# Performance work log

Measured on AMD Instinct MI355X. Metric: run time of the kernel, lower is better.

Reference implementation:

```python
import jax, jax.numpy as jnp
import numpy as np

B, H, S, D = 4, 16, 2048, 64


def setup_inputs() -> dict:
    key = jax.random.key(0)
    kq, kk, kv = jax.random.split(key, 3)
    q = jax.random.normal(kq, (B, H, S, D), dtype=jnp.float32)
    k = jax.random.normal(kk, (B, H, S, D), dtype=jnp.float32)
    v = jax.random.normal(kv, (B, H, S, D), dtype=jnp.float32)
    return {"q": q, "k": k, "v": v, "num_k": 170}


def reference(q, k, v, num_k):
    d_tensor = k.shape[-1]
    # [B,H,S,S] score matrix
    score = jnp.einsum("bhqd,bhkd->bhqk", q, k) / jnp.sqrt(jnp.float32(d_tensor))
    nk = min(int(num_k), k.shape[2])
    if nk:
        # kth-largest value per query row acts as threshold
        top_vals = jax.lax.top_k(score, nk)[0]          # [B,H,S,nk]
        thresh = top_vals[..., -1:]                      # [B,H,S,1]
        score = jnp.where(score < thresh, jnp.float32(-1e18), score)
    attn = jax.nn.softmax(score, axis=-1)
    return jnp.einsum("bhqk,bhkd->bhqd", attn, v)
```

## Files before the change

### kernel.cpp

```cpp
#include <hip/hip_runtime.h>
#include <math.h>

#define S_LEN 2048
#define DHEAD 64
#define NBINS 512
#define BPL (NBINS / 64)
#define CANDMAX 48
#define NBH 64
#define NROWS (NBH * S_LEN)
#define VT_BYTES (64ull * DHEAD * S_LEN * 2)

typedef _Float16 f16x8 __attribute__((ext_vector_type(8)));
typedef _Float16 f16x4 __attribute__((ext_vector_type(4)));
typedef float    f32x4 __attribute__((ext_vector_type(4)));

__global__ __launch_bounds__(256)
void prep_vt(const float* __restrict__ V, _Float16* __restrict__ VT) {
  const int bh  = (int)blockIdx.x >> 3;
  const int dg8 = (int)blockIdx.x & 7;
  const int t   = (int)threadIdx.x;
  const int dim = dg8 * 8 + (t >> 5);
  const int kc  = t & 31;
  const float* Vb = V + (size_t)bh * (S_LEN * DHEAD);
  _Float16* VTb = VT + ((size_t)bh * DHEAD + dim) * S_LEN;
  for (int i = 0; i < 8; ++i) {
    int key0 = (kc + i * 32) * 8;
    f16x8 h;
    #pragma unroll
    for (int j = 0; j < 8; ++j)
      h[j] = (_Float16)Vb[(size_t)(key0 + j) * DHEAD + dim];
    *(f16x8*)(VTb + key0) = h;
  }
}

__global__ __launch_bounds__(256, 4)
void qk_kernel(const float* __restrict__ Q, const float* __restrict__ K,
               float* __restrict__ Sws, int row0) {
  __shared__ __align__(16) char kbuf[32768];
  f16x8* Khw = (f16x8*)kbuf;
  f16x8* Klw = (f16x8*)(kbuf + 16384);

  const int tid  = (int)threadIdx.x;
  const int lane = tid & 63;
  const int wid  = tid >> 6;
  const int nxl  = (int)gridDim.x >> 3;
  const int xcd  = (int)blockIdx.x & 7;
  const int lb   = (int)blockIdx.x >> 3;
  const int rb   = lb >> 2;
  const int kb   = lb & 3;
  const int rowl = xcd * (nxl * 16) + rb * 64 + wid * 16;
  const int rowg = row0 + rowl;
  const int bh   = rowg >> 11;
  const int key0 = kb * 512;

  const int g = lane >> 4;
  const int m = lane & 15;

  f16x8 a_hi0, a_lo0, a_hi1, a_lo1;
  {
    const float* Qrow = Q + (size_t)(rowg + m) * DHEAD;
    float4 qa = *(const float4*)(Qrow + g * 8);
    float4 qb = *(const float4*)(Qrow + g * 8 + 4);
    float4 qc = *(const float4*)(Qrow + 32 + g * 8);
    float4 qd = *(const float4*)(Qrow + 32 + g * 8 + 4);
    float x[16] = {qa.x,qa.y,qa.z,qa.w, qb.x,qb.y,qb.z,qb.w,
                   qc.x,qc.y,qc.z,qc.w, qd.x,qd.y,qd.z,qd.w};
    #pragma unroll
    for (int j = 0; j < 8; ++j) {
      _Float16 h0 = (_Float16)x[j];
      a_hi0[j] = h0;  a_lo0[j] = (_Float16)(x[j] - (float)h0);
      _Float16 h1 = (_Float16)x[8 + j];
      a_hi1[j] = h1;  a_lo1[j] = (_Float16)(x[8 + j] - (float)h1);
    }
  }

  const float* Kb = K + (size_t)bh * (S_LEN * DHEAD);
  float* Srow = Sws + (size_t)rowl * S_LEN;

  const int skey  = tid >> 1;
  const int shalf = tid & 1;
  const int ssw   = skey & 7;

  float4 pf[8];
  {
    const float4* kr = (const float4*)(Kb + (size_t)(key0 + skey) * DHEAD + shalf * 32);
    #pragma unroll
    for (int j = 0; j < 8; ++j) pf[j] = kr[j];
  }

  for (int t = 0; t < 4; ++t) {
    #pragma unroll
    for (int jj = 0; jj < 4; ++jj) {
      float x[8] = {pf[2*jj].x, pf[2*jj].y, pf[2*jj].z, pf[2*jj].w,
                    pf[2*jj+1].x, pf[2*jj+1].y, pf[2*jj+1].z, pf[2*jj+1].w};
      f16x8 hi, lo;
      #pragma unroll
      for (int j = 0; j < 8; ++j) {
        _Float16 h = (_Float16)x[j];
        hi[j] = h;
        lo[j] = (_Float16)(x[j] - (float)h);
      }
      int c = shalf * 4 + jj;
      Khw[skey * 8 + (c ^ ssw)] = hi;
      Klw[skey * 8 + (c ^ ssw)] = lo;
    }
    if (t + 1 < 4) {
      const float4* kr = (const float4*)(Kb + (size_t)(key0 + (t + 1) * 128 + skey) * DHEAD + shalf * 32);
      #pragma unroll
      for (int j = 0; j < 8; ++j) pf[j] = kr[j];
    }
    __syncthreads();

    const f16x8* Kh = (const f16x8*)kbuf;
    const f16x8* Kl = (const f16x8*)(kbuf + 16384);
    int slot0 = ( g      ^ (m & 7));
    int slot1 = ((4 + g) ^ (m & 7));
    #pragma unroll
    for (int p = 0; p < 8; ++p) {
      int keyr = p * 16 + m;
      f16x8 b_hi0 = Kh[keyr * 8 + slot0];
      f16x8 b_hi1 = Kh[keyr * 8 + slot1];
      f16x8 b_lo0 = Kl[keyr * 8 + slot0];
      f16x8 b_lo1 = Kl[keyr * 8 + slot1];
      f32x4 acc = {0.f, 0.f, 0.f, 0.f};
      acc = __builtin_amdgcn_mfma_f32_16x16x32_f16(a_hi0, b_hi0, acc, 0, 0, 0);
      acc = __builtin_amdgcn_mfma_f32_16x16x32_f16(a_hi1, b_hi1, acc, 0, 0, 0);
      acc = __builtin_amdgcn_mfma_f32_16x16x32_f16(a_hi0, b_lo0, acc, 0, 0, 0);
      acc = __builtin_amdgcn_mfma_f32_16x16x32_f16(a_hi1, b_lo1, acc, 0, 0, 0);
      acc = __builtin_amdgcn_mfma_f32_16x16x32_f16(a_lo0, b_hi0, acc, 0, 0, 0);
      acc = __builtin_amdgcn_mfma_f32_16x16x32_f16(a_lo1, b_hi1, acc, 0, 0, 0);
      acc = __builtin_amdgcn_mfma_f32_16x16x32_f16(a_lo0, b_lo0, acc, 0, 0, 0);
      acc = __builtin_amdgcn_mfma_f32_16x16x32_f16(a_lo1, b_lo1, acc, 0, 0, 0);
      int col = key0 + t * 128 + p * 16 + m;
      #pragma unroll
      for (int rg = 0; rg < 4; ++rg)
        __builtin_nontemporal_store(acc[rg] * 0.125f,
            &Srow[(size_t)(g * 4 + rg) * S_LEN + col]);
    }
    __syncthreads();
  }
}

__global__ __launch_bounds__(512, 4)
void selmm_kernel(const float* __restrict__ Sws, const _Float16* __restrict__ VT,
                  const int* __restrict__ nkp, float* __restrict__ Out, int row0) {
  __shared__ __align__(16) char pbuf[65536];
  __shared__ __align__(16) float4 redS[4][64];
  __shared__ float psumS[16];
  __shared__ unsigned candCnt[8];
  unsigned* histS = (unsigned*)pbuf;
  float*    candA = (float*)(pbuf + 16384);

  const int tid  = (int)threadIdx.x;
  const int lane = tid & 63;
  const int wid  = tid >> 6;
  const int nxl  = (int)gridDim.x >> 3;
  const int xcd  = (int)blockIdx.x & 7;
  const int lbk  = (int)blockIdx.x >> 3;
  const int rowlb = xcd * (nxl * 16) + lbk * 16;
  const int rowgb = row0 + rowlb;
  const int bh    = rowgb >> 11;

  int nk = nkp[0];
  if (nk > S_LEN) nk = S_LEN;

  unsigned* hw = histS + wid * NBINS;
  float*    cw = candA + wid * CANDMAX;
  float sarr[2][32];
  float thr2[2], vmx2[2];

  #pragma unroll
  for (int rr = 0; rr < 2; ++rr) {
    const int rloc = wid * 2 + rr;
    {
      const f32x4* S4 = (const f32x4*)(Sws + (size_t)(rowlb + rloc) * S_LEN);
      #pragma unroll
      for (int j = 0; j < 8; ++j) {
        f32x4 v4 = __builtin_nontemporal_load(S4 + j * 64 + lane);
        sarr[rr][j*4+0] = v4[0]; sarr[rr][j*4+1] = v4[1];
        sarr[rr][j*4+2] = v4[2]; sarr[rr][j*4+3] = v4[3];
      }
    }

    float vmax = -INFINITY, vmin = INFINITY;
    #pragma unroll
    for (int q = 0; q < 32; ++q) {
      vmax = fmaxf(vmax, sarr[rr][q]); vmin = fminf(vmin, sarr[rr][q]);
    }
    #pragma unroll
    for (int off = 32; off >= 1; off >>= 1) {
      vmax = fmaxf(vmax, __shfl_xor(vmax, off));
      vmin = fminf(vmin, __shfl_xor(vmin, off));
    }

    float thresh = -INFINITY;
    if (nk > 0) {
      float range = vmax - vmin;
      float scale = (range > 0.f) ? ((float)NBINS / range) : 0.f;
      float boff  = vmin * scale;

      #pragma unroll
      for (int i2 = 0; i2 < BPL; ++i2) hw[(i2 << 6) | lane] = 0u;
      #pragma unroll
      for (int q = 0; q < 32; ++q) {
        int bb = (int)fmaf(sarr[rr][q], scale, -boff);
        bb = bb < 0 ? 0 : (bb > NBINS - 1 ? NBINS - 1 : bb);
        atomicAdd(&hw[((bb & 7) << 6) | (bb >> 3)], 1u);
      }

      unsigned A = 0;
      #pragma unroll
      for (int i2 = 0; i2 < BPL; ++i2) A += hw[(i2 << 6) | lane];
      unsigned ssum = A;
      #pragma unroll
      for (int off = 1; off <= 32; off <<= 1) {
        unsigned u = (unsigned)__shfl_down((int)ssum, off);
        if (lane + off < 64) ssum += u;
      }
      unsigned cum = ssum - A;
      int bsel = -1; int mloc = 0; int nbloc = 0;
      #pragma unroll
      for (int i2 = BPL - 1; i2 >= 0; --i2) {
        unsigned c0 = cum; cum += hw[(i2 << 6) | lane];
        if (bsel < 0 && c0 < (unsigned)nk && cum >= (unsigned)nk) {
          bsel = (lane << 3) | i2; mloc = nk - (int)c0; nbloc = (int)(cum - c0);
        }
      }
      unsigned long long fm = __ballot(bsel >= 0);
      int srcl = __ffsll(fm) - 1;
      bsel = __shfl(bsel, srcl);
      int mth  = __shfl(mloc, srcl);
      int nbin = __shfl(nbloc, srcl);

      if (nbin <= CANDMAX) {
        if (lane == 0) candCnt[wid] = 0u;
        __builtin_amdgcn_wave_barrier();
        #pragma unroll
        for (int q = 0; q < 32; ++q) {
          int bb = (int)fmaf(sarr[rr][q], scale, -boff);
          bb = bb < 0 ? 0 : (bb > NBINS - 1 ? NBINS - 1 : bb);
          if (bb == bsel) {
            unsigned ix = atomicAdd(&candCnt[wid], 1u);
            if (ix < CANDMAX) cw[ix] = sarr[rr][q];
          }
        }
        __builtin_amdgcn_wave_barrier();
        float prev = INFINITY, kth = -INFINITY;
        int got = 0, guard = 0;
        while (got < mth && guard++ <= CANDMAX) {
          float best = -INFINITY;
          for (int i = 0; i < nbin; ++i) {
            float v = cw[i];
            if (v < prev && v > best) best = v;
          }
          int ce = 0;
          for (int i = 0; i < nbin; ++i) if (cw[i] == best) ce++;
          got += ce; prev = best; kth = best;
        }
        thresh = kth;
      } else {
        unsigned inbin = 0;
        #pragma unroll
        for (int q = 0; q < 32; ++q) {
          int bb = (int)fmaf(sarr[rr][q], scale, -boff);
          bb = bb < 0 ? 0 : (bb > NBINS - 1 ? NBINS - 1 : bb);
          if (bb == bsel) inbin |= (1u << q);
        }
        while (true) {
          float cmax = -INFINITY;
          #pragma unroll
          for (int q = 0; q < 32; ++q) if (inbin & (1u << q)) cmax = fmaxf(cmax, sarr[rr][q]);
          #pragma unroll
          for (int off = 32; off >= 1; off >>= 1) cmax = fmaxf(cmax, __shfl_xor(cmax, off));
          int cnt = 0;
          #pragma unroll
          for (int q = 0; q < 32; ++q) if ((inbin & (1u << q)) && sarr[rr][q] == cmax) cnt++;
          #pragma unroll
          for (int off = 32; off >= 1; off >>= 1) cnt += __shfl_xor(cnt, off);
          if (mth <= cnt) { thresh = cmax; break; }
          mth -= cnt;
          #pragma unroll
          for (int q = 0; q < 32; ++q) if ((inbin & (1u << q)) && sarr[rr][q] == cmax) inbin &= ~(1u << q);
        }
      }
    }
    thr2[rr] = thresh; vmx2[rr] = vmax;

    float psum = 0.f;
    #pragma unroll
    for (int q = 0; q < 32; ++q) {
      float s = sarr[rr][q];
      psum += (s >= thresh) ? __expf(s - vmax) : 0.f;
    }
    #pragma unroll
    for (int off = 32; off >= 1; off >>= 1) psum += __shfl_xor(psum, off);
    if (lane == 0) psumS[rloc] = psum;
  }
  __syncthreads();

  #pragma unroll
  for (int rr = 0; rr < 2; ++rr) {
    const int row = wid * 2 + rr;
    const int swz = (row & 7) << 4;
    #pragma unroll
    for (int j = 0; j < 8; ++j) {
      f16x4 pv;
      #pragma unroll
      for (int c = 0; c < 4; ++c) {
        float s = sarr[rr][j*4+c];
        pv[c] = (_Float16)((s >= thr2[rr]) ? __expf(s - vmx2[rr]) : 0.f);
      }
      *(f16x4*)(pbuf + ((row * 4096 + j * 512 + lane * 8) ^ swz)) = pv;
    }
  }
  __syncthreads();

  const int g    = lane >> 4;
  const int n16  = lane & 15;
  const int dg   = wid & 3;
  const int kh   = wid >> 2;
  const int swzA = (n16 & 7) << 4;
  const _Float16* VTb = VT + (size_t)bh * (DHEAD * S_LEN);
  f32x4 acc = {0.f, 0.f, 0.f, 0.f};

  #pragma unroll
  for (int kt = 0; kt < 8; ++kt) {
    #pragma unroll
    for (int s = 0; s < 4; ++s) {
      f16x8 af = *(const f16x8*)(pbuf +
          ((n16 * 4096 + kt * 512 + kh * 256 + s * 64 + g * 16) ^ swzA));
      f16x8 bf = *(const f16x8*)(VTb + (size_t)(dg * 16 + n16) * S_LEN +
                                 kt * 256 + kh * 128 + s * 32 + g * 8);
      acc = __builtin_amdgcn_mfma_f32_16x16x32_f16(af, bf, acc, 0, 0, 0);
    }
  }

  if (kh == 1) {
    redS[dg][lane] = make_float4(acc[0], acc[1], acc[2], acc[3]);
  }
  __syncthreads();
  if (kh == 0) {
    float4 o = redS[dg][lane];
    float ov[4] = {o.x, o.y, o.z, o.w};
    #pragma unroll
    for (int rg = 0; rg < 4; ++rg) {
      int row = g * 4 + rg;
      float val = (acc[rg] + ov[rg]) / psumS[row];
      Out[(size_t)(rowgb + row) * DHEAD + dg * 16 + n16] = val;
    }
  }
}

#define TQ 16
#define KT 128
#define NTILES (S_LEN / KT)
#define THREADS 512
#define LCAP 256
#define SOFF   0
#define KHI    131072
#define KLO    147456
#define HOFF   131072
#define KLOFF  147456
#define PLOFF  155648

__global__ __launch_bounds__(THREADS, 2)
void dpsa_kernel(const float* __restrict__ Q, const float* __restrict__ K,
                 const float* __restrict__ V, const int* __restrict__ nkp,
                 float* __restrict__ Out) {
  __shared__ __align__(16) char smem[163840];
  float* Sf = (float*)(smem + SOFF);

  const int tid  = (int)threadIdx.x;
  const int lane = tid & 63;
  const int wid  = tid >> 6;
  const int bid  = (int)blockIdx.x;
  const int bh   = bid >> 7;
  const int qblk = bid & 127;
  const size_t base = (size_t)bh * (size_t)(S_LEN * DHEAD);
  const float* Kbh = K + base;
  const float* Vbh = V + base;

  int nk = nkp[0];
  if (nk > S_LEN) nk = S_LEN;

  const int g = lane >> 4;
  const int m = lane & 15;

  f16x8 a_hi0, a_lo0, a_hi1, a_lo1;
  {
    const float* Qrow = Q + base + (size_t)(qblk * TQ + m) * DHEAD;
    float4 qa = *(const float4*)(Qrow + g * 8);
    float4 qb = *(const float4*)(Qrow + g * 8 + 4);
    float4 qc = *(const float4*)(Qrow + 32 + g * 8);
    float4 qd = *(const float4*)(Qrow + 32 + g * 8 + 4);
    float x[16] = {qa.x,qa.y,qa.z,qa.w, qb.x,qb.y,qb.z,qb.w,
                   qc.x,qc.y,qc.z,qc.w, qd.x,qd.y,qd.z,qd.w};
    #pragma unroll
    for (int j = 0; j < 8; ++j) {
      _Float16 h0 = (_Float16)x[j];
      a_hi0[j] = h0;  a_lo0[j] = (_Float16)(x[j] - (float)h0);
      _Float16 h1 = (_Float16)x[8 + j];
      a_hi1[j] = h1;  a_lo1[j] = (_Float16)(x[8 + j] - (float)h1);
    }
  }

  const f16x8* Kh = (const f16x8*)(smem + KHI);
  const f16x8* Kl = (const f16x8*)(smem + KLO);
  const int keyl = tid >> 2;
  const int q4i  = tid & 3;
  const int sw   = keyl & 7;

  float4 pf0, pf1, pf2, pf3;
  {
    const float4* Kg4 = (const float4*)Kbh;
    int idx = keyl * 16 + q4i * 4;
    pf0 = Kg4[idx]; pf1 = Kg4[idx + 1]; pf2 = Kg4[idx + 2]; pf3 = Kg4[idx + 3];
  }

  for (int t = 0; t < NTILES; ++t) {
    {
      float x[16] = {pf0.x,pf0.y,pf0.z,pf0.w, pf1.x,pf1.y,pf1.z,pf1.w,
                     pf2.x,pf2.y,pf2.z,pf2.w, pf3.x,pf3.y,pf3.z,pf3.w};
      f16x8 hi0, hi1, lo0, lo1;
      #pragma unroll
      for (int j = 0; j < 8; ++j) {
        _Float16 h0 = (_Float16)x[j];
        hi0[j] = h0;  lo0[j] = (_Float16)(x[j] - (float)h0);
        _Float16 h1 = (_Float16)x[8 + j];
        hi1[j] = h1;  lo1[j] = (_Float16)(x[8 + j] - (float)h1);
      }
      f16x8* KhwF = (f16x8*)(smem + KHI);
      f16x8* KlwF = (f16x8*)(smem + KLO);
      KhwF[keyl * 8 + ((q4i * 2)     ^ sw)] = hi0;
      KhwF[keyl * 8 + ((q4i * 2 + 1) ^ sw)] = hi1;
      KlwF[keyl * 8 + ((q4i * 2)     ^ sw)] = lo0;
      KlwF[keyl * 8 + ((q4i * 2 + 1) ^ sw)] = lo1;
    }
    if (t + 1 < NTILES) {
      const float4* Kg4 = (const float4*)(Kbh + (size_t)(t + 1) * (KT * DHEAD));
      int idx = keyl * 16 + q4i * 4;
      pf0 = Kg4[idx]; pf1 = Kg4[idx + 1]; pf2 = Kg4[idx + 2]; pf3 = Kg4[idx + 3];
    }
    __syncthreads();
    {
      int keyr = wid * 16 + m;
      int s0 = ( g      ^ (m & 7));
      int s1 = ((4 + g) ^ (m & 7));
      f16x8 b_hi0 = Kh[keyr * 8 + s0];
      f16x8 b_hi1 = Kh[keyr * 8 + s1];
      f16x8 b_lo0 = Kl[keyr * 8 + s0];
      f16x8 b_lo1 = Kl[keyr * 8 + s1];
      f32x4 acc = {0.f, 0.f, 0.f, 0.f};
      acc = __builtin_amdgcn_mfma_f32_16x16x32_f16(a_hi0, b_hi0, acc, 0, 0, 0);
      acc = __builtin_amdgcn_mfma_f32_16x16x32_f16(a_hi1, b_hi1, acc, 0, 0, 0);
      acc = __builtin_amdgcn_mfma_f32_16x16x32_f16(a_hi0, b_lo0, acc, 0, 0, 0);
      acc = __builtin_amdgcn_mfma_f32_16x16x32_f16(a_hi1, b_lo1, acc, 0, 0, 0);
      acc = __builtin_amdgcn_mfma_f32_16x16x32_f16(a_lo0, b_hi0, acc, 0, 0, 0);
      acc = __builtin_amdgcn_mfma_f32_16x16x32_f16(a_lo1, b_hi1, acc, 0, 0, 0);
      int keyabs = t * KT + wid * 16 + m;
      #pragma unroll
      for (int rg = 0; rg < 4; ++rg)
        Sf[(size_t)(g * 4 + rg) * S_LEN + keyabs] = acc[rg] * 0.125f;
    }
    __syncthreads();
  }

  unsigned* hw = (unsigned*)(smem + HOFF)  + wid * NBINS;
  unsigned* kl = (unsigned*)(smem + KLOFF) + wid * LCAP;
  float*    pl = (float*)(smem + PLOFF)    + wid * LCAP;
  const float4* S4 = (const float4*)(smem + SOFF);

  for (int rr = 0; rr < 2; ++rr) {
    const int row = wid * 2 + rr;
    float sarr[32];
    #pragma unroll
    for (int j = 0; j < 8; ++j) {
      float4 v4 = S4[row * (S_LEN / 4) + j * 64 + lane];
      sarr[j*4+0] = v4.x; sarr[j*4+1] = v4.y;
      sarr[j*4+2] = v4.z; sarr[j*4+3] = v4.w;
    }

    float vmax = -INFINITY, vmin = INFINITY;
    #pragma unroll
    for (int q = 0; q < 32; ++q) {
      vmax = fmaxf(vmax, sarr[q]); vmin = fminf(vmin, sarr[q]);
    }
    #pragma unroll
    for (int off = 32; off >= 1; off >>= 1) {
      vmax = fmaxf(vmax, __shfl_xor(vmax, off));
      vmin = fminf(vmin, __shfl_xor(vmin, off));
    }

    float thresh = -INFINITY;
    if (nk > 0) {
      float range = vmax - vmin;
      float scale = (range > 0.f) ? ((float)NBINS / range) : 0.f;
      #pragma unroll
      for (int i2 = 0; i2 < BPL; ++i2) hw[(i2 << 6) | lane] = 0u;
      #pragma unroll
      for (int q = 0; q < 32; ++q) {
        int bb = (int)((sarr[q] - vmin) * scale);
        bb = bb < 0 ? 0 : (bb > NBINS - 1 ? NBINS - 1 : bb);
        atomicAdd(&hw[((bb & 7) << 6) | (bb >> 3)], 1u);
      }
      unsigned A = 0; unsigned hv[BPL];
      #pragma unroll
      for (int i2 = 0; i2 < BPL; ++i2) { hv[i2] = hw[(i2 << 6) | lane]; A += hv[i2]; }
      unsigned ssum = A;
      #pragma unroll
      for (int off = 1; off <= 32; off <<= 1) {
        unsigned u = (unsigned)__shfl_down((int)ssum, off);
        if (lane + off < 64) ssum += u;
      }
      unsigned cum = ssum - A;
      int bsel = -1; int mloc = 0;
      #pragma unroll
      for (int i2 = BPL - 1; i2 >= 0; --i2) {
        unsigned c0 = cum; cum += hv[i2];
        if (bsel < 0 && c0 < (unsigned)nk && cum >= (unsigned)nk) {
          bsel = (lane << 3) | i2; mloc = nk - (int)c0;
        }
      }
      unsigned long long fm = __ballot(bsel >= 0);
      int srcl = __ffsll(fm) - 1;
      bsel = __shfl(bsel, srcl);
      int mth = __shfl(mloc, srcl);

      unsigned inbin = 0;
      #pragma unroll
      for (int q = 0; q < 32; ++q) {
        int bb = (int)((sarr[q] - vmin) * scale);
        bb = bb < 0 ? 0 : (bb > NBINS - 1 ? NBINS - 1 : bb);
        if (bb == bsel) inbin |= (1u << q);
      }
      while (true) {
        float cmax = -INFINITY;
        #pragma unroll
        for (int q = 0; q < 32; ++q) if (inbin & (1u << q)) cmax = fmaxf(cmax, sarr[q]);
        #pragma unroll
        for (int off = 32; off >= 1; off >>= 1) cmax = fmaxf(cmax, __shfl_xor(cmax, off));
        int cnt = 0;
        #pragma unroll
        for (int q = 0; q < 32; ++q) if ((inbin & (1u << q)) && sarr[q] == cmax) cnt++;
        #pragma unroll
        for (int off = 32; off >= 1; off >>= 1) cnt += __shfl_xor(cnt, off);
        if (mth <= cnt) { thresh = cmax; break; }
        mth -= cnt;
        #pragma unroll
        for (int q = 0; q < 32; ++q) if ((inbin & (1u << q)) && sarr[q] == cmax) inbin &= ~(1u << q);
      }
    }

    float psum = 0.f;
    #pragma unroll
    for (int q = 0; q < 32; ++q) {
      float p = (sarr[q] >= thresh) ? expf(sarr[q] - vmax) : 0.f;
      sarr[q] = p; psum += p;
    }
    #pragma unroll
    for (int off = 32; off >= 1; off >>= 1) psum += __shfl_xor(psum, off);

    unsigned nkept = 0;
    #pragma unroll
    for (int q = 0; q < 32; ++q) {
      bool keep = sarr[q] > 0.f;
      unsigned long long mk = __ballot(keep);
      if (keep) {
        unsigned idx = nkept + (unsigned)__popcll(mk & ((1ull << lane) - 1ull));
        if (idx < LCAP) {
          kl[idx] = (unsigned)((q >> 2) * 256 + lane * 4 + (q & 3));
          pl[idx] = sarr[q];
        }
      }
      nkept += (unsigned)__popcll(mk);
    }

    float acc0 = 0.f, acc1 = 0.f, acc2 = 0.f, acc3 = 0.f;
    if (nkept <= LCAP) {
      unsigned i = 0;
      for (; i + 4 <= nkept; i += 4) {
        acc0 = fmaf(pl[i+0], Vbh[(size_t)kl[i+0] * DHEAD + lane], acc0);
        acc1 = fmaf(pl[i+1], Vbh[(size_t)kl[i+1] * DHEAD + lane], acc1);
        acc2 = fmaf(pl[i+2], Vbh[(size_t)kl[i+2] * DHEAD + lane], acc2);
        acc3 = fmaf(pl[i+3], Vbh[(size_t)kl[i+3] * DHEAD + lane], acc3);
      }
      for (; i < nkept; ++i)
        acc0 = fmaf(pl[i], Vbh[(size_t)kl[i] * DHEAD + lane], acc0);
    } else {
      #pragma unroll
      for (int q = 0; q < 32; ++q) {
        for (int sl = 0; sl < 64; ++sl) {
          float pp = __shfl(sarr[q], sl);
          if (pp > 0.f)
            acc0 = fmaf(pp, Vbh[(size_t)((q >> 2) * 256 + sl * 4 + (q & 3)) * DHEAD + lane], acc0);
        }
      }
    }
    float accv = (acc0 + acc1) + (acc2 + acc3);
    Out[base + (size_t)(qblk * TQ + row) * DHEAD + lane] = accv / psum;
  }
}

extern "C" void kernel_launch(void* const* d_in, const int* in_sizes, int n_in,
                              void* d_out, int out_size, void* d_ws, size_t ws_size,
                              hipStream_t stream) {
  const float* q  = (const float*)d_in[0];
  const float* k  = (const float*)d_in[1];
  const float* v  = (const float*)d_in[2];
  const int*   nk = (const int*)d_in[3];
  float* out = (float*)d_out;

  size_t srem = (ws_size > VT_BYTES) ? (ws_size - VT_BYTES) : 0;
  size_t maxrows = srem / ((size_t)S_LEN * sizeof(float));
  long long chunk = (long long)(maxrows / 512) * 512;
  if (chunk > NROWS) chunk = NROWS;

  if (chunk >= 512) {
    _Float16* vt = (_Float16*)d_ws;
    float* sws = (float*)((char*)d_ws + VT_BYTES);
    prep_vt<<<dim3(512), dim3(256), 0, stream>>>(v, vt);
    for (int row0 = 0; row0 < NROWS; row0 += (int)chunk) {
      int rows = (NROWS - row0 < (int)chunk) ? (NROWS - row0) : (int)chunk;
      qk_kernel<<<dim3(rows / 16), dim3(256), 0, stream>>>(q, k, sws, row0);
      selmm_kernel<<<dim3(rows / 16), dim3(512), 0, stream>>>(sws, vt, nk, out, row0);
    }
  } else {
    dpsa_kernel<<<dim3(8192), dim3(THREADS), 0, stream>>>(q, k, v, nk, out);
  }
}
```

Measured before the change: 988.8 us.

## Process 8 rows per selmm block, one row per wave, to cut registers and LDS

The selection+PV kernel now assigns one score row per wave (8 rows per block) instead of two, halving the per-thread score array and shrinking LDS from 64KB to 36KB. The grid doubles to keep coverage. The 16-row MFMA tile is padded with a zeroed row, so half the PV MFMA work and V loads per block are wasted. The aim is higher occupancy and more latency hiding in the memory-bound selection phase, paid for with duplicated V reads.

```diff
diff --git a/kernel.cpp b/kernel.cpp
--- a/kernel.cpp
+++ b/kernel.cpp
@@ -144,9 +144,9 @@
 __global__ __launch_bounds__(512, 4)
 void selmm_kernel(const float* __restrict__ Sws, const _Float16* __restrict__ VT,
                   const int* __restrict__ nkp, float* __restrict__ Out, int row0) {
-  __shared__ __align__(16) char pbuf[65536];
+  __shared__ __align__(16) char pbuf[36864];
   __shared__ __align__(16) float4 redS[4][64];
-  __shared__ float psumS[16];
+  __shared__ float psumS[8];
   __shared__ unsigned candCnt[8];
   unsigned* histS = (unsigned*)pbuf;
   float*    candA = (float*)(pbuf + 16384);
@@ -157,7 +157,7 @@
   const int nxl  = (int)gridDim.x >> 3;
   const int xcd  = (int)blockIdx.x & 7;
   const int lbk  = (int)blockIdx.x >> 3;
-  const int rowlb = xcd * (nxl * 16) + lbk * 16;
+  const int rowlb = xcd * (nxl * 8) + lbk * 8;
   const int rowgb = row0 + rowlb;
   const int bh    = rowgb >> 11;
 
@@ -166,151 +166,153 @@
 
   unsigned* hw = histS + wid * NBINS;
   float*    cw = candA + wid * CANDMAX;
-  float sarr[2][32];
-  float thr2[2], vmx2[2];
-
+  float sarr[32];
+  float thr, vmx;
+
+  {
+    const f32x4* S4 = (const f32x4*)(Sws + (size_t)(rowlb + wid) * S_LEN);
+    #pragma unroll
+    for (int j = 0; j < 8; ++j) {
+      f32x4 v4 = __builtin_nontemporal_load(S4 + j * 64 + lane);
+      sarr[j*4+0] = v4[0]; sarr[j*4+1] = v4[1];
+      sarr[j*4+2] = v4[2]; sarr[j*4+3] = v4[3];
+    }
+  }
+
+  float vmax = -INFINITY, vmin = INFINITY;
   #pragma unroll
-  for (int rr = 0; rr < 2; ++rr) {
-    const int rloc = wid * 2 + rr;
-    {
-      const f32x4* S4 = (const f32x4*)(Sws + (size_t)(rowlb + rloc) * S_LEN);
-      #pragma unroll
-      for (int j = 0; j < 8; ++j) {
-        f32x4 v4 = __builtin_nontemporal_load(S4 + j * 64 + lane);
-        sarr[rr][j*4+0] = v4[0]; sarr[rr][j*4+1] = v4[1];
-        sarr[rr][j*4+2] = v4[2]; sarr[rr][j*4+3] = v4[3];
-      }
-    }
-
-    float vmax = -INFINITY, vmin = INFINITY;
+  for (int q = 0; q < 32; ++q) {
+    vmax = fmaxf(vmax, sarr[q]); vmin = fminf(vmin, sarr[q]);
+  }
+  #pragma unroll
+  for (int off = 32; off >= 1; off >>= 1) {
+    vmax = fmaxf(vmax, __shfl_xor(vmax, off));
+    vmin = fminf(vmin, __shfl_xor(vmin, off));
+  }
+
+  float thresh = -INFINITY;
+  if (nk > 0) {
+    float range = vmax - vmin;
+    float scale = (range > 0.f) ? ((float)NBINS / range) : 0.f;
+    float boff  = vmin * scale;
+
+    #pragma unroll
+    for (int i2 = 0; i2 < BPL; ++i2) hw[(i2 << 6) | lane] = 0u;
     #pragma unroll
     for (int q = 0; q < 32; ++q) {
-      vmax = fmaxf(vmax, sarr[rr][q]); vmin = fminf(vmin, sarr[rr][q]);
-    }
-    #pragma unroll
-    for (int off = 32; off >= 1; off >>= 1) {
-      vmax = fmaxf(vmax, __shfl_xor(vmax, off));
-      vmin = fminf(vmin, __shfl_xor(vmin, off));
-    }
-
-    float thresh = -INFINITY;
-    if (nk > 0) {
-      float range = vmax - vmin;
-      float scale = (range > 0.f) ? ((float)NBINS / range) : 0.f;
-      float boff  = vmin * scale;
-
-      #pragma unroll
-      for (int i2 = 0; i2 < BPL; ++i2) hw[(i2 << 6) | lane] = 0u;
+      int bb = (int)fmaf(sarr[q], scale, -boff);
+      bb = bb < 0 ? 0 : (bb > NBINS - 1 ? NBINS - 1 : bb);
+      atomicAdd(&hw[((bb & 7) << 6) | (bb >> 3)], 1u);
+    }
+
+    unsigned A = 0;
+    #pragma unroll
+    for (int i2 = 0; i2 < BPL; ++i2) A += hw[(i2 << 6) | lane];
+    unsigned ssum = A;
+    #pragma unroll
+    for (int off = 1; off <= 32; off <<= 1) {
+      unsigned u = (unsigned)__shfl_down((int)ssum, off);
+      if (lane + off < 64) ssum += u;
+    }
+    unsigned cum = ssum - A;
+    int bsel = -1; int mloc = 0; int nbloc = 0;
+    #pragma unroll
+    for (int i2 = BPL - 1; i2 >= 0; --i2) {
+      unsigned c0 = cum; cum += hw[(i2 << 6) | lane];
+      if (bsel < 0 && c0 < (unsigned)nk && cum >= (unsigned)nk) {
+        bsel = (lane << 3) | i2; mloc = nk - (int)c0; nbloc = (int)(cum - c0);
+      }
+    }
+    unsigned long long fm = __ballot(bsel >= 0);
+    int srcl = __ffsll(fm) - 1;
+    bsel = __shfl(bsel, srcl);
+    int mth  = __shfl(mloc, srcl);
+    int nbin = __shfl(nbloc, srcl);
+
+    if (nbin <= CANDMAX) {
+      if (lane == 0) candCnt[wid] = 0u;
+      __builtin_amdgcn_wave_barrier();
       #pragma unroll
       for (int q = 0; q < 32; ++q) {
-        int bb = (int)fmaf(sarr[rr][q], scale, -boff);
+        int bb = (int)fmaf(sarr[q], scale, -boff);
         bb = bb < 0 ? 0 : (bb > NBINS - 1 ? NBINS - 1 : bb);
-        atomicAdd(&hw[((bb & 7) << 6) | (bb >> 3)], 1u);
-      }
-
-      unsigned A = 0;
-      #pragma unroll
-      for (int i2 = 0; i2 < BPL; ++i2) A += hw[(i2 << 6) | lane];
-      unsigned ssum = A;
-      #pragma unroll
-      for (int off = 1; off <= 32; off <<= 1) {
-        unsigned u = (unsigned)__shfl_down((int)ssum, off);
-        if (lane + off < 64) ssum += u;
-      }
-      unsigned cum = ssum - A;
-      int bsel = -1; int mloc = 0; int nbloc = 0;
-      #pragma unroll
-      for (int i2 = BPL - 1; i2 >= 0; --i2) {
-        unsigned c0 = cum; cum += hw[(i2 << 6) | lane];
-        if (bsel < 0 && c0 < (unsigned)nk && cum >= (unsigned)nk) {
-          bsel = (lane << 3) | i2; mloc = nk - (int)c0; nbloc = (int)(cum - c0);
+        if (bb == bsel) {
+          unsigned ix = atomicAdd(&candCnt[wid], 1u);
+          if (ix < CANDMAX) cw[ix] = sarr[q];
         }
       }
-      unsigned long long fm = __ballot(bsel >= 0);
-      int srcl = __ffsll(fm) - 1;
-      bsel = __shfl(bsel, srcl);
-      int mth  = __shfl(mloc, srcl);
-      int nbin = __shfl(nbloc, srcl);
-
-      if (nbin <= CANDMAX) {
-        if (lane == 0) candCnt[wid] = 0u;
-        __builtin_amdgcn_wave_barrier();
-        #pragma unroll
-        for (int q = 0; q < 32; ++q) {
-          int bb = (int)fmaf(sarr[rr][q], scale, -boff);
-          bb = bb < 0 ? 0 : (bb > NBINS - 1 ? NBINS - 1 : bb);
-          if (bb == bsel) {
-            unsigned ix = atomicAdd(&candCnt[wid], 1u);
-            if (ix < CANDMAX) cw[ix] = sarr[rr][q];
-          }
+      __builtin_amdgcn_wave_barrier();
+      float prev = INFINITY, kth = -INFINITY;
+      int got = 0, guard = 0;
+      while (got < mth && guard++ <= CANDMAX) {
+        float best = -INFINITY;
+        for (int i = 0; i < nbin; ++i) {
+          float v = cw[i];
+          if (v < prev && v > best) best = v;
         }
-        __builtin_amdgcn_wave_barrier();
-        float prev = INFINITY, kth = -INFINITY;
-        int got = 0, guard = 0;
-        while (got < mth && guard++ <= CANDMAX) {
-          float best = -INFINITY;
-          for (int i = 0; i < nbin; ++i) {
-            float v = cw[i];
-            if (v < prev && v > best) best = v;
-          }
-          int ce = 0;
-          for (int i = 0; i < nbin; ++i) if (cw[i] == best) ce++;
-          got += ce; prev = best; kth = best;
-        }
-        thresh = kth;
-      } else {
-        unsigned inbin = 0;
-        #pragma unroll
-        for (int q = 0; q < 32; ++q) {
-          int bb = (int)fmaf(sarr[rr][q], scale, -boff);
-          bb = bb < 0 ? 0 : (bb > NBINS - 1 ? NBINS - 1 : bb);
-          if (bb == bsel) inbin |= (1u << q);
-        }
-        while (true) {
-          float cmax = -INFINITY;
-          #pragma unroll
-          for (int q = 0; q < 32; ++q) if (inbin & (1u << q)) cmax = fmaxf(cmax, sarr[rr][q]);
-          #pragma unroll
-          for (int off = 32; off >= 1; off >>= 1) cmax = fmaxf(cmax, __shfl_xor(cmax, off));
-          int cnt = 0;
-          #pragma unroll
-          for (int q = 0; q < 32; ++q) if ((inbin & (1u << q)) && sarr[rr][q] == cmax) cnt++;
-          #pragma unroll
-          for (int off = 32; off >= 1; off >>= 1) cnt += __shfl_xor(cnt, off);
-          if (mth <= cnt) { thresh = cmax; break; }
-          mth -= cnt;
-          #pragma unroll
-          for (int q = 0; q < 32; ++q) if ((inbin & (1u << q)) && sarr[rr][q] == cmax) inbin &= ~(1u << q);
-        }
-      }
-    }
-    thr2[rr] = thresh; vmx2[rr] = vmax;
-
+        int ce = 0;
+        for (int i = 0; i < nbin; ++i) if (cw[i] == best) ce++;
+        got += ce; prev = best; kth = best;
+      }
+      thresh = kth;
+    } else {
+      unsigned inbin = 0;
+      #pragma unroll
+      for (int q = 0; q < 32; ++q) {
+        int bb = (int)fmaf(sarr[q], scale, -boff);
+        bb = bb < 0 ? 0 : (bb > NBINS - 1 ? NBINS - 1 : bb);
+        if (bb == bsel) inbin |= (1u << q);
+      }
+      while (true) {
+        float cmax = -INFINITY;
+        #pragma unroll
+        for (int q = 0; q < 32; ++q) if (inbin & (1u << q)) cmax = fmaxf(cmax, sarr[q]);
+        #pragma unroll
+        for (int off = 32; off >= 1; off >>= 1) cmax = fmaxf(cmax, __shfl_xor(cmax, off));
+        int cnt = 0;
+        #pragma unroll
+        for (int q = 0; q < 32; ++q) if ((inbin & (1u << q)) && sarr[q] == cmax) cnt++;
+        #pragma unroll
+        for (int off = 32; off >= 1; off >>= 1) cnt += __shfl_xor(cnt, off);
+        if (mth <= cnt) { thresh = cmax; break; }
+        mth -= cnt;
+        #pragma unroll
+        for (int q = 0; q < 32; ++q) if ((inbin & (1u << q)) && sarr[q] == cmax) inbin &= ~(1u << q);
+      }
+    }
+  }
+  thr = thresh; vmx = vmax;
+
+  {
     float psum = 0.f;
     #pragma unroll
     for (int q = 0; q < 32; ++q) {
-      float s = sarr[rr][q];
-      psum += (s >= thresh) ? __expf(s - vmax) : 0.f;
+      float s = sarr[q];
+      psum += (s >= thr) ? __expf(s - vmx) : 0.f;
     }
     #pragma unroll
     for (int off = 32; off >= 1; off >>= 1) psum += __shfl_xor(psum, off);
-    if (lane == 0) psumS[rloc] = psum;
+    if (lane == 0) psumS[wid] = psum;
   }
   __syncthreads();
 
-  #pragma unroll
-  for (int rr = 0; rr < 2; ++rr) {
-    const int row = wid * 2 + rr;
-    const int swz = (row & 7) << 4;
+  {
+    const int swz = (wid & 7) << 4;
     #pragma unroll
     for (int j = 0; j < 8; ++j) {
       f16x4 pv;
       #pragma unroll
       for (int c = 0; c < 4; ++c) {
-        float s = sarr[rr][j*4+c];
-        pv[c] = (_Float16)((s >= thr2[rr]) ? __expf(s - vmx2[rr]) : 0.f);
-      }
-      *(f16x4*)(pbuf + ((row * 4096 + j * 512 + lane * 8) ^ swz)) = pv;
+        float s = sarr[j*4+c];
+        pv[c] = (_Float16)((s >= thr) ? __expf(s - vmx) : 0.f);
+      }
+      *(f16x4*)(pbuf + ((wid * 4096 + j * 512 + lane * 8) ^ swz)) = pv;
+    }
+    if (wid == 0) {
+      f16x4 z = {(_Float16)0.f, (_Float16)0.f, (_Float16)0.f, (_Float16)0.f};
+      #pragma unroll
+      for (int j = 0; j < 8; ++j)
+        *(f16x4*)(pbuf + (8 * 4096 + j * 512 + lane * 8)) = z;
     }
   }
   __syncthreads();
@@ -319,7 +321,8 @@
   const int n16  = lane & 15;
   const int dg   = wid & 3;
   const int kh   = wid >> 2;
-  const int swzA = (n16 & 7) << 4;
+  const int prow = (n16 < 8) ? n16 : 8;
+  const int swzA = (prow & 7) << 4;
   const _Float16* VTb = VT + (size_t)bh * (DHEAD * S_LEN);
   f32x4 acc = {0.f, 0.f, 0.f, 0.f};
 
@@ -328,7 +331,7 @@
     #pragma unroll
     for (int s = 0; s < 4; ++s) {
       f16x8 af = *(const f16x8*)(pbuf +
-          ((n16 * 4096 + kt * 512 + kh * 256 + s * 64 + g * 16) ^ swzA));
+          ((prow * 4096 + kt * 512 + kh * 256 + s * 64 + g * 16) ^ swzA));
       f16x8 bf = *(const f16x8*)(VTb + (size_t)(dg * 16 + n16) * S_LEN +
                                  kt * 256 + kh * 128 + s * 32 + g * 8);
       acc = __builtin_amdgcn_mfma_f32_16x16x32_f16(af, bf, acc, 0, 0, 0);
@@ -345,8 +348,10 @@
     #pragma unroll
     for (int rg = 0; rg < 4; ++rg) {
       int row = g * 4 + rg;
-      float val = (acc[rg] + ov[rg]) / psumS[row];
-      Out[(size_t)(rowgb + row) * DHEAD + dg * 16 + n16] = val;
+      if (row < 8) {
+        float val = (acc[rg] + ov[rg]) / psumS[row];
+        Out[(size_t)(rowgb + row) * DHEAD + dg * 16 + n16] = val;
+      }
     }
   }
 }
@@ -622,7 +627,7 @@
     for (int row0 = 0; row0 < NROWS; row0 += (int)chunk) {
       int rows = (NROWS - row0 < (int)chunk) ? (NROWS - row0) : (int)chunk;
       qk_kernel<<<dim3(rows / 16), dim3(256), 0, stream>>>(q, k, sws, row0);
-      selmm_kernel<<<dim3(rows / 16), dim3(512), 0, stream>>>(sws, vt, nk, out, row0);
+      selmm_kernel<<<dim3(rows / 8), dim3(512), 0, stream>>>(sws, vt, nk, out, row0);
     }
   } else {
     dpsa_kernel<<<dim3(8192), dim3(THREADS), 0, stream>>>(q, k, v, nk, out);
```

After: 1.195 ms. 20.9% more time.
